# Kernel optimization log

Measured on AMD Instinct MI355X. Metric: run time of the kernel, lower is better.

## Reference

```python
import jax, jax.numpy as jnp
import numpy as np
import math

B, N, D, H = 32, 512, 512, 8
DK = D // H
MAX_DIST = 100.0
BINS = 20
BIN_SIZE = MAX_DIST / BINS


def setup_inputs() -> dict:
    key = jax.random.key(0)
    ks = jax.random.split(key, 12)
    s = 1.0 / math.sqrt(D)
    inp = {
        "x": jax.random.normal(ks[0], (B, N, D), dtype=jnp.float32),
        "distance_matrix": jax.random.uniform(ks[1], (B, N, N), dtype=jnp.float32) * MAX_DIST,
        "Wq": jax.random.uniform(ks[2], (D, D), jnp.float32, -s, s),
        "bq": jax.random.uniform(ks[3], (D,), jnp.float32, -s, s),
        "Wk": jax.random.uniform(ks[4], (D, D), jnp.float32, -s, s),
        "bk": jax.random.uniform(ks[5], (D,), jnp.float32, -s, s),
        "Wv": jax.random.uniform(ks[6], (D, D), jnp.float32, -s, s),
        "bv": jax.random.uniform(ks[7], (D,), jnp.float32, -s, s),
        "Wo": jax.random.uniform(ks[8], (D, D), jnp.float32, -s, s),
        "bo": jax.random.uniform(ks[9], (D,), jnp.float32, -s, s),
        "dist_weights": jnp.ones((BINS + 1,), dtype=jnp.float32),
    }
    return inp


def reference(x, distance_matrix, Wq, bq, Wk, bk, Wv, bv, Wo, bo, dist_weights):
    temperature = 1.0
    # Linear projections; torch nn.Linear computes x @ W.T + b
    q = (x @ Wq.T + bq).reshape(B, N, H, DK).transpose(0, 2, 1, 3)  # [B,H,N,DK]
    k = (x @ Wk.T + bk).reshape(B, N, H, DK).transpose(0, 2, 1, 3)
    v = (x @ Wv.T + bv).reshape(B, N, H, DK).transpose(0, 2, 1, 3)

    scores = jnp.einsum("bhqd,bhkd->bhqk", q, k) / math.sqrt(DK)  # [B,H,N,N]

    # Relative position bias: bin distances, look up scalar weight per pair
    binned = jnp.clip((distance_matrix / BIN_SIZE).astype(jnp.int32), 0, BINS)  # [B,N,N]
    bias = dist_weights[binned] / temperature  # [B,N,N]
    scores = scores + bias[:, None, :, :]  # broadcast over heads

    attn = jax.nn.softmax(scores, axis=-1)  # dropout is identity in eval
    out = jnp.einsum("bhqk,bhkd->bhqd", attn, v)  # [B,H,N,DK]
    out = out.transpose(0, 2, 1, 3).reshape(B, N, D)
    return out @ Wo.T + bo
```

## Files before the change

kernel.cpp:

```cpp
#include <hip/hip_runtime.h>
#include <hip/hip_fp16.h>
#include <math.h>
#include <stdint.h>

#define BB 32
#define NN 512
#define DDIM 512
#define HH 8
#define DK 64

typedef __attribute__((ext_vector_type(8))) short short8;
typedef __attribute__((ext_vector_type(4))) float floatx4;
typedef unsigned short ushort_t;
typedef unsigned int uint_t;

__device__ __forceinline__ void gl_lds16(const void* g, void* l) {
    __builtin_amdgcn_global_load_lds(
        (const __attribute__((address_space(1))) uint_t*)g,
        (__attribute__((address_space(3))) uint_t*)l,
        16, 0, 0);
}

__device__ __forceinline__ ushort_t f2bf(float f) {
    uint_t u = __builtin_bit_cast(uint_t, f);
    u += 0x7fff + ((u >> 16) & 1);
    return (ushort_t)(u >> 16);
}

__device__ __forceinline__ uint_t pkbf(float a, float b) {
    return (uint_t)f2bf(a) | ((uint_t)f2bf(b) << 16);
}

__device__ __forceinline__ float h2f(ushort_t u) {
    return __half2float(__ushort_as_half(u));
}

__global__ __launch_bounds__(256) void cvt_bf16(const float* __restrict__ s,
                                                ushort_t* __restrict__ d, int n8) {
    const int i = blockIdx.x * 256 + threadIdx.x;
    if (i >= n8) return;
    const float4 a = ((const float4*)s)[i * 2 + 0];
    const float4 b = ((const float4*)s)[i * 2 + 1];
    uint4 o;
    o.x = pkbf(a.x, a.y); o.y = pkbf(a.z, a.w);
    o.z = pkbf(b.x, b.y); o.w = pkbf(b.z, b.w);
    *(uint4*)(d + i * 8) = o;
}

__global__ __launch_bounds__(256) void cvt_w4(
    const float* __restrict__ w0, const float* __restrict__ w1,
    const float* __restrict__ w2, const float* __restrict__ w3,
    ushort_t* __restrict__ o0, ushort_t* __restrict__ o1,
    ushort_t* __restrict__ o2, ushort_t* __restrict__ o3) {
    const float* s; ushort_t* d;
    if (blockIdx.y == 0)      { s = w0; d = o0; }
    else if (blockIdx.y == 1) { s = w1; d = o1; }
    else if (blockIdx.y == 2) { s = w2; d = o2; }
    else                      { s = w3; d = o3; }
    const int i = blockIdx.x * 256 + threadIdx.x;
    const float4 a = ((const float4*)s)[i * 2 + 0];
    const float4 b = ((const float4*)s)[i * 2 + 1];
    uint4 o;
    o.x = pkbf(a.x, a.y); o.y = pkbf(a.z, a.w);
    o.z = pkbf(b.x, b.y); o.w = pkbf(b.z, b.w);
    *(uint4*)(d + i * 8) = o;
}

__global__ __launch_bounds__(256) void bias_half(const float* __restrict__ dist,
                                                 const float* __restrict__ dw,
                                                 ushort_t* __restrict__ T, int n8) {
    __shared__ float dws[21];
    if (threadIdx.x < 21) dws[threadIdx.x] = (dw[threadIdx.x] - 3.0f) * 1.44269504f;
    __syncthreads();
    const int i = blockIdx.x * 256 + threadIdx.x;
    if (i >= n8) return;
    float dv[8];
    { const float4 a = ((const float4*)dist)[i * 2 + 0];
      const float4 b = ((const float4*)dist)[i * 2 + 1];
      dv[0]=a.x; dv[1]=a.y; dv[2]=a.z; dv[3]=a.w;
      dv[4]=b.x; dv[5]=b.y; dv[6]=b.z; dv[7]=b.w; }
    ushort_t h[8];
    #pragma unroll
    for (int j = 0; j < 8; ++j) {
        int bin = (int)(dv[j] / 5.0f);
        bin = bin < 0 ? 0 : (bin > 20 ? 20 : bin);
        h[j] = __half_as_ushort(__float2half(dws[bin]));
    }
    uint4 o;
    o.x = (uint_t)h[0] | ((uint_t)h[1] << 16);
    o.y = (uint_t)h[2] | ((uint_t)h[3] << 16);
    o.z = (uint_t)h[4] | ((uint_t)h[5] << 16);
    o.w = (uint_t)h[6] | ((uint_t)h[7] << 16);
    *(uint4*)(T + i * 8) = o;
}

__global__ __launch_bounds__(256) void transp_v(const ushort_t* __restrict__ V,
                                                ushort_t* __restrict__ Vt) {
    __shared__ ushort_t T[64][72];
    const int tid = threadIdx.x;
    const int q0 = blockIdx.x * 64;
    const int bh = blockIdx.y, b = bh >> 3, h = bh & 7;
    #pragma unroll
    for (int rnd = 0; rnd < 2; ++rnd) {
        const int idx = rnd * 256 + tid;
        const int row = idx >> 3, c8 = (idx & 7) * 8;
        const uint4 v = *(const uint4*)&V[((size_t)(b * NN + q0 + row)) * DDIM + h * DK + c8];
        ushort_t* t = &T[row][c8];
        t[0] = (ushort_t)v.x; t[1] = (ushort_t)(v.x >> 16);
        t[2] = (ushort_t)v.y; t[3] = (ushort_t)(v.y >> 16);
        t[4] = (ushort_t)v.z; t[5] = (ushort_t)(v.z >> 16);
        t[6] = (ushort_t)v.w; t[7] = (ushort_t)(v.w >> 16);
    }
    __syncthreads();
    #pragma unroll
    for (int rnd = 0; rnd < 2; ++rnd) {
        const int idx = rnd * 256 + tid;
        const int d = idx >> 3, q8 = (idx & 7) * 8;
        uint4 o;
        o.x = (uint_t)T[q8 + 0][d] | ((uint_t)T[q8 + 1][d] << 16);
        o.y = (uint_t)T[q8 + 2][d] | ((uint_t)T[q8 + 3][d] << 16);
        o.z = (uint_t)T[q8 + 4][d] | ((uint_t)T[q8 + 5][d] << 16);
        o.w = (uint_t)T[q8 + 6][d] | ((uint_t)T[q8 + 7][d] << 16);
        *(uint4*)&Vt[((size_t)(bh * DK + d)) * NN + q0 + q8] = o;
    }
}

#define GEMM_CORE(Aptr, Wptr)                                                           \
    __shared__ ushort_t As[128 * 32];                                                   \
    __shared__ ushort_t Bs[128 * 32];                                                   \
    const int tid = threadIdx.x;                                                        \
    const int lane = tid & 63, wid = tid >> 6;                                          \
    const int quad = lane >> 4, l15 = lane & 15;                                        \
    const int m0 = blockIdx.x * 128, n0 = blockIdx.y * 128;                             \
    const int wy = wid >> 1, wx = wid & 1;                                              \
    floatx4 acc[4][4];                                                                  \
    _Pragma("unroll") for (int i = 0; i < 4; ++i)                                       \
        _Pragma("unroll") for (int j = 0; j < 4; ++j)                                   \
            _Pragma("unroll") for (int r = 0; r < 4; ++r) acc[i][j][r] = 0.f;           \
    for (int k0 = 0; k0 < DDIM; k0 += 32) {                                             \
        __syncthreads();                                                                \
        _Pragma("unroll") for (int j = 0; j < 4; ++j) {                                 \
            const int t = wid * 4 + j;                                                  \
            const int rowi = ((t & 7) << 4) + (lane >> 2);                              \
            const int cd = (lane & 3) ^ ((rowi >> 1) & 3);                              \
            if (t < 8)                                                                  \
                gl_lds16(Aptr + (size_t)(m0 + rowi) * DDIM + k0 + cd * 8,               \
                         (char*)As + ((t & 7) << 10));                                  \
            else                                                                        \
                gl_lds16(Wptr + (size_t)(n0 + rowi) * DDIM + k0 + cd * 8,               \
                         (char*)Bs + ((t & 7) << 10));                                  \
        }                                                                               \
        __syncthreads();                                                                \
        short8 aw[4], bt[4];                                                            \
        _Pragma("unroll") for (int fi = 0; fi < 4; ++fi) {                              \
            const int r = wy * 64 + fi * 16 + l15;                                      \
            aw[fi] = *(const short8*)((const char*)Bs + r * 64 +                        \
                                      ((quad ^ ((r >> 1) & 3)) << 4));                  \
        }                                                                               \
        _Pragma("unroll") for (int ti = 0; ti < 4; ++ti) {                              \
            const int r = wx * 64 + ti * 16 + l15;                                      \
            bt[ti] = *(const short8*)((const char*)As + r * 64 +                        \
                                      ((quad ^ ((r >> 1) & 3)) << 4));                  \
        }                                                                               \
        _Pragma("unroll") for (int fi = 0; fi < 4; ++fi)                                \
            _Pragma("unroll") for (int ti = 0; ti < 4; ++ti)                            \
                acc[fi][ti] = __builtin_amdgcn_mfma_f32_16x16x32_bf16(                  \
                    aw[fi], bt[ti], acc[fi][ti], 0, 0, 0);                              \
    }

__global__ __launch_bounds__(256) void gemm_qkv(
    const ushort_t* __restrict__ A,
    const ushort_t* __restrict__ W0, const ushort_t* __restrict__ W1,
    const ushort_t* __restrict__ W2,
    const float* __restrict__ b0, const float* __restrict__ b1,
    const float* __restrict__ b2,
    ushort_t* __restrict__ o0, ushort_t* __restrict__ o1, ushort_t* __restrict__ o2) {
    const ushort_t* W; const float* bias; ushort_t* dst;
    if (blockIdx.z == 0)      { W = W0; bias = b0; dst = o0; }
    else if (blockIdx.z == 1) { W = W1; bias = b1; dst = o1; }
    else                      { W = W2; bias = b2; dst = o2; }
    GEMM_CORE(A, W)
    #pragma unroll
    for (int fi = 0; fi < 4; ++fi) {
        const int f = n0 + wy * 64 + fi * 16 + quad * 4;
        const float4 b4 = *(const float4*)&bias[f];
        #pragma unroll
        for (int ti = 0; ti < 4; ++ti) {
            const int token = m0 + wx * 64 + ti * 16 + l15;
            uint2 v;
            v.x = pkbf(acc[fi][ti][0] + b4.x, acc[fi][ti][1] + b4.y);
            v.y = pkbf(acc[fi][ti][2] + b4.z, acc[fi][ti][3] + b4.w);
            *(uint2*)&dst[(size_t)token * DDIM + f] = v;
        }
    }
}

__global__ __launch_bounds__(256) void gemm_out(
    const ushort_t* __restrict__ A, const ushort_t* __restrict__ Wo,
    const float* __restrict__ bo, float* __restrict__ dst) {
    GEMM_CORE(A, Wo)
    #pragma unroll
    for (int fi = 0; fi < 4; ++fi) {
        const int f = n0 + wy * 64 + fi * 16 + quad * 4;
        const float4 b4 = *(const float4*)&bo[f];
        #pragma unroll
        for (int ti = 0; ti < 4; ++ti) {
            const int token = m0 + wx * 64 + ti * 16 + l15;
            float4 v;
            v.x = acc[fi][ti][0] + b4.x; v.y = acc[fi][ti][1] + b4.y;
            v.z = acc[fi][ti][2] + b4.z; v.w = acc[fi][ti][3] + b4.w;
            *(float4*)&dst[(size_t)token * DDIM + f] = v;
        }
    }
}

__global__ __launch_bounds__(256) void attn_mfma(
    const ushort_t* __restrict__ Qg, const ushort_t* __restrict__ Kg,
    const ushort_t* __restrict__ Vtg, const ushort_t* __restrict__ Tg,
    ushort_t* __restrict__ aout) {
    __shared__ ushort_t Ks[64 * 64];
    __shared__ ushort_t Vs[64 * 64];
    __shared__ ushort_t Ps[64 * 64];

    const int tid = threadIdx.x, lane = tid & 63, wid = tid >> 6;
    const int quad = lane >> 4, l15 = lane & 15;
    const int q0 = blockIdx.x * 64, h = blockIdx.y, b = blockIdx.z;
    const int qrow = q0 + wid * 16 + l15;
    const float K1 = 0.18033688f;

    const ushort_t* qp = Qg + (size_t)(b * NN + qrow) * DDIM + h * DK;
    short8 bq[2];
    #pragma unroll
    for (int ks = 0; ks < 2; ++ks)
        bq[ks] = *(const short8*)(qp + ks * 32 + quad * 8);

    const ushort_t* trow = Tg + (size_t)(b * NN + qrow) * NN;
    const int prow = wid * 16 + l15;
    const int swk = l15 & 7;

    floatx4 O[4];
    #pragma unroll
    for (int ni = 0; ni < 4; ++ni)
        #pragma unroll
        for (int r = 0; r < 4; ++r) O[ni][r] = 0.f;
    float lsum = 0.f;

    for (int kt = 0; kt < 8; ++kt) {
        const int k0 = kt * 64;
        __syncthreads();
        #pragma unroll
        for (int j = 0; j < 2; ++j) {
            const int t = wid * 2 + j;
            const int row = t * 8 + (lane >> 3);
            const int cd = (lane & 7) ^ (row & 7) ^ ((row >> 3) & 7);
            gl_lds16(Kg + (size_t)(b * NN + k0 + row) * DDIM + h * DK + cd * 8,
                     (char*)Ks + t * 1024);
            gl_lds16(Vtg + ((size_t)((b * HH + h) * DK + row)) * NN + k0 + cd * 8,
                     (char*)Vs + t * 1024);
        }
        uint2 tv[4];
        #pragma unroll
        for (int f = 0; f < 4; ++f)
            tv[f] = *(const uint2*)(trow + k0 + f * 16 + quad * 4);
        __syncthreads();

        floatx4 S[4];
        #pragma unroll
        for (int f = 0; f < 4; ++f)
            #pragma unroll
            for (int r = 0; r < 4; ++r) S[f][r] = 0.f;
        #pragma unroll
        for (int ks = 0; ks < 2; ++ks) {
            #pragma unroll
            for (int f = 0; f < 4; ++f) {
                const int r = f * 16 + l15;
                const int ch = (ks * 4 + quad) ^ (r & 7) ^ ((r >> 3) & 7);
                const short8 ak = *(const short8*)((const char*)Ks + r * 128 + (ch << 4));
                S[f] = __builtin_amdgcn_mfma_f32_16x16x32_bf16(ak, bq[ks], S[f], 0, 0, 0);
            }
        }

        #pragma unroll
        for (int f = 0; f < 4; ++f) {
            const float t0 = h2f((ushort_t)(tv[f].x));
            const float t1 = h2f((ushort_t)(tv[f].x >> 16));
            const float t2 = h2f((ushort_t)(tv[f].y));
            const float t3 = h2f((ushort_t)(tv[f].y >> 16));
            const float p0 = exp2f(S[f][0] * K1 + t0);
            const float p1 = exp2f(S[f][1] * K1 + t1);
            const float p2 = exp2f(S[f][2] * K1 + t2);
            const float p3 = exp2f(S[f][3] * K1 + t3);
            lsum += (p0 + p1) + (p2 + p3);
            uint2 pw;
            pw.x = pkbf(p0, p1);
            pw.y = pkbf(p2, p3);
            *(uint2*)((char*)Ps + prow * 128 + (((f * 4 + quad) ^ (swk << 1)) << 3)) = pw;
        }

        #pragma unroll
        for (int ks = 0; ks < 2; ++ks) {
            const int chp = ((ks * 4 + quad) ^ swk) << 4;
            const short8 bp = *(const short8*)((const char*)Ps + prow * 128 + chp);
            #pragma unroll
            for (int ni = 0; ni < 4; ++ni) {
                const int rv = ni * 16 + l15;
                const int chv = (ks * 4 + quad) ^ (rv & 7) ^ ((rv >> 3) & 7);
                const short8 av = *(const short8*)((const char*)Vs + rv * 128 + (chv << 4));
                O[ni] = __builtin_amdgcn_mfma_f32_16x16x32_bf16(av, bp, O[ni], 0, 0, 0);
            }
        }
    }

    lsum += __shfl_xor(lsum, 16);
    lsum += __shfl_xor(lsum, 32);
    const float inv = 1.0f / lsum;
    #pragma unroll
    for (int ni = 0; ni < 4; ++ni) {
        uint2 ov;
        ov.x = pkbf(O[ni][0] * inv, O[ni][1] * inv);
        ov.y = pkbf(O[ni][2] * inv, O[ni][3] * inv);
        *(uint2*)&aout[(size_t)(b * NN + qrow) * DDIM + h * DK + ni * 16 + quad * 4] = ov;
    }
}

extern "C" void kernel_launch(void* const* d_in, const int* in_sizes, int n_in,
                              void* d_out, int out_size, void* d_ws, size_t ws_size,
                              hipStream_t stream) {
    const float* x    = (const float*)d_in[0];
    const float* dist = (const float*)d_in[1];
    const float* Wq   = (const float*)d_in[2];
    const float* bq   = (const float*)d_in[3];
    const float* Wk   = (const float*)d_in[4];
    const float* bk   = (const float*)d_in[5];
    const float* Wv   = (const float*)d_in[6];
    const float* bv   = (const float*)d_in[7];
    const float* Wo   = (const float*)d_in[8];
    const float* bo   = (const float*)d_in[9];
    const float* dw   = (const float*)d_in[10];
    float* out = (float*)d_out;

    const size_t NELT = (size_t)BB * NN * DDIM;
    ushort_t* xb  = (ushort_t*)d_ws;
    ushort_t* wqb = xb + NELT;
    ushort_t* wkb = wqb + DDIM * DDIM;
    ushort_t* wvb = wkb + DDIM * DDIM;
    ushort_t* wob = wvb + DDIM * DDIM;
    ushort_t* qb  = wob + DDIM * DDIM;
    ushort_t* kb  = qb + NELT;
    ushort_t* vb  = kb + NELT;
    ushort_t* vt  = vb + NELT;
    ushort_t* Tm  = vt + NELT;
    ushort_t* ab  = xb;

    cvt_bf16<<<4096, 256, 0, stream>>>(x, xb, (int)(NELT / 8));
    cvt_w4<<<dim3(128, 4), 256, 0, stream>>>(Wq, Wk, Wv, Wo, wqb, wkb, wvb, wob);
    bias_half<<<4096, 256, 0, stream>>>(dist, dw, Tm, (int)(NELT / 8));

    gemm_qkv<<<dim3(128, 4, 3), 256, 0, stream>>>(xb, wqb, wkb, wvb, bq, bk, bv,
                                                  qb, kb, vb);
    transp_v<<<dim3(8, 256), 256, 0, stream>>>(vb, vt);
    attn_mfma<<<dim3(8, 8, 32), 256, 0, stream>>>(qb, kb, vt, Tm, ab);
    gemm_out<<<dim3(128, 4), 256, 0, stream>>>(ab, wob, bo, out);
}
```

Before: 250.0 us.

## Fuse attention per batch-head with full K/V resident in LDS and fp16 PV

Rewrites attention so each block handles one (batch, head) with 512 threads, loading all K and transposed V into shared memory once, then each wave processes 64 queries without per-tile barriers. V projection output and softmax probabilities switch to fp16 so the PV product uses f16 MFMA. This removes redundant K/V reloads and synchronisation across query tiles, at the cost of large LDS use (one block per CU), high register pressure, and an unoverlapped upfront load.

Measured after the change: 245.8 us. No clear change (-1.7%).

```diff
diff --git a/kernel.cpp b/kernel.cpp
--- a/kernel.cpp
+++ b/kernel.cpp
@@ -10,6 +10,8 @@
 #define DK 64
 
 typedef __attribute__((ext_vector_type(8))) short short8;
+typedef __attribute__((ext_vector_type(8))) _Float16 half8;
+typedef __attribute__((ext_vector_type(2))) _Float16 half2v;
 typedef __attribute__((ext_vector_type(4))) float floatx4;
 typedef unsigned short ushort_t;
 typedef unsigned int uint_t;
@@ -29,6 +31,10 @@
 
 __device__ __forceinline__ uint_t pkbf(float a, float b) {
     return (uint_t)f2bf(a) | ((uint_t)f2bf(b) << 16);
+}
+
+__device__ __forceinline__ uint_t pkh(float a, float b) {
+    return __builtin_bit_cast(uint_t, __builtin_amdgcn_cvt_pkrtz(a, b));
 }
 
 __device__ __forceinline__ float h2f(ushort_t u) {
@@ -179,6 +185,7 @@
     if (blockIdx.z == 0)      { W = W0; bias = b0; dst = o0; }
     else if (blockIdx.z == 1) { W = W1; bias = b1; dst = o1; }
     else                      { W = W2; bias = b2; dst = o2; }
+    const bool as_f16 = (blockIdx.z == 2);
     GEMM_CORE(A, W)
     #pragma unroll
     for (int fi = 0; fi < 4; ++fi) {
@@ -187,9 +194,11 @@
         #pragma unroll
         for (int ti = 0; ti < 4; ++ti) {
             const int token = m0 + wx * 64 + ti * 16 + l15;
+            const float v0 = acc[fi][ti][0] + b4.x, v1 = acc[fi][ti][1] + b4.y;
+            const float v2 = acc[fi][ti][2] + b4.z, v3 = acc[fi][ti][3] + b4.w;
             uint2 v;
-            v.x = pkbf(acc[fi][ti][0] + b4.x, acc[fi][ti][1] + b4.y);
-            v.y = pkbf(acc[fi][ti][2] + b4.z, acc[fi][ti][3] + b4.w);
+            if (as_f16) { v.x = pkh(v0, v1);  v.y = pkh(v2, v3); }
+            else        { v.x = pkbf(v0, v1); v.y = pkbf(v2, v3); }
             *(uint2*)&dst[(size_t)token * DDIM + f] = v;
         }
     }
@@ -214,112 +223,152 @@
     }
 }
 
-__global__ __launch_bounds__(256) void attn_mfma(
+__global__ __launch_bounds__(512, 2) void attn_fused(
     const ushort_t* __restrict__ Qg, const ushort_t* __restrict__ Kg,
     const ushort_t* __restrict__ Vtg, const ushort_t* __restrict__ Tg,
     ushort_t* __restrict__ aout) {
-    __shared__ ushort_t Ks[64 * 64];
-    __shared__ ushort_t Vs[64 * 64];
-    __shared__ ushort_t Ps[64 * 64];
+    __shared__ ushort_t Ks[512 * 64];
+    __shared__ ushort_t Vs[64 * 512];
+    __shared__ ushort_t Ps[8 * 1024];
 
     const int tid = threadIdx.x, lane = tid & 63, wid = tid >> 6;
     const int quad = lane >> 4, l15 = lane & 15;
-    const int q0 = blockIdx.x * 64, h = blockIdx.y, b = blockIdx.z;
-    const int qrow = q0 + wid * 16 + l15;
+    const int h = blockIdx.x, b = blockIdx.y;
     const float K1 = 0.18033688f;
 
-    const ushort_t* qp = Qg + (size_t)(b * NN + qrow) * DDIM + h * DK;
-    short8 bq[2];
-    #pragma unroll
-    for (int ks = 0; ks < 2; ++ks)
-        bq[ks] = *(const short8*)(qp + ks * 32 + quad * 8);
-
-    const ushort_t* trow = Tg + (size_t)(b * NN + qrow) * NN;
-    const int prow = wid * 16 + l15;
+    #pragma unroll
+    for (int j = 0; j < 8; ++j) {
+        const int t = wid * 8 + j;
+        {
+            const int row = t * 8 + (lane >> 3);
+            const int key = (row & 7) ^ ((row >> 3) & 7);
+            const int g = (lane & 7) ^ key;
+            gl_lds16(Kg + (size_t)(b * NN + row) * DDIM + h * DK + g * 8,
+                     (char*)Ks + t * 1024);
+        }
+        {
+            const int key = (t & 7) ^ ((t >> 3) & 7);
+            const int g = lane ^ key;
+            gl_lds16(Vtg + (size_t)((b * HH + h) * DK + t) * NN + g * 8,
+                     (char*)Vs + t * 1024);
+        }
+    }
+
+    short8 bq[4][2];
+    #pragma unroll
+    for (int qs = 0; qs < 4; ++qs) {
+        const ushort_t* qp =
+            Qg + (size_t)(b * NN + wid * 64 + qs * 16 + l15) * DDIM + h * DK;
+        bq[qs][0] = *(const short8*)(qp + quad * 8);
+        bq[qs][1] = *(const short8*)(qp + 32 + quad * 8);
+    }
+
+    float lsum[4] = {0.f, 0.f, 0.f, 0.f};
+    floatx4 O[4][4];
+    #pragma unroll
+    for (int qs = 0; qs < 4; ++qs)
+        #pragma unroll
+        for (int ni = 0; ni < 4; ++ni)
+            #pragma unroll
+            for (int r = 0; r < 4; ++r) O[qs][ni][r] = 0.f;
+
+    char* const pbase = (char*)Ps + wid * 2048;
     const int swk = l15 & 7;
 
-    floatx4 O[4];
-    #pragma unroll
-    for (int ni = 0; ni < 4; ++ni)
-        #pragma unroll
-        for (int r = 0; r < 4; ++r) O[ni][r] = 0.f;
-    float lsum = 0.f;
+    __syncthreads();
 
     for (int kt = 0; kt < 8; ++kt) {
-        const int k0 = kt * 64;
-        __syncthreads();
-        #pragma unroll
-        for (int j = 0; j < 2; ++j) {
-            const int t = wid * 2 + j;
-            const int row = t * 8 + (lane >> 3);
-            const int cd = (lane & 7) ^ (row & 7) ^ ((row >> 3) & 7);
-            gl_lds16(Kg + (size_t)(b * NN + k0 + row) * DDIM + h * DK + cd * 8,
-                     (char*)Ks + t * 1024);
-            gl_lds16(Vtg + ((size_t)((b * HH + h) * DK + row)) * NN + k0 + cd * 8,
-                     (char*)Vs + t * 1024);
-        }
-        uint2 tv[4];
-        #pragma unroll
-        for (int f = 0; f < 4; ++f)
-            tv[f] = *(const uint2*)(trow + k0 + f * 16 + quad * 4);
-        __syncthreads();
-
-        floatx4 S[4];
-        #pragma unroll
-        for (int f = 0; f < 4; ++f)
-            #pragma unroll
-            for (int r = 0; r < 4; ++r) S[f][r] = 0.f;
-        #pragma unroll
-        for (int ks = 0; ks < 2; ++ks) {
+        uint2 tv[4][4];
+        #pragma unroll
+        for (int qs = 0; qs < 4; ++qs) {
+            const ushort_t* tp =
+                Tg + (size_t)(b * NN + wid * 64 + qs * 16 + l15) * NN + kt * 64;
+            #pragma unroll
+            for (int f = 0; f < 4; ++f)
+                tv[qs][f] = *(const uint2*)(tp + f * 16 + quad * 4);
+        }
+        short8 kf[2][4];
+        #pragma unroll
+        for (int ks = 0; ks < 2; ++ks)
             #pragma unroll
             for (int f = 0; f < 4; ++f) {
-                const int r = f * 16 + l15;
-                const int ch = (ks * 4 + quad) ^ (r & 7) ^ ((r >> 3) & 7);
-                const short8 ak = *(const short8*)((const char*)Ks + r * 128 + (ch << 4));
-                S[f] = __builtin_amdgcn_mfma_f32_16x16x32_bf16(ak, bq[ks], S[f], 0, 0, 0);
+                const int row = kt * 64 + f * 16 + l15;
+                const int key = (row & 7) ^ ((row >> 3) & 7);
+                kf[ks][f] = *(const short8*)((const char*)Ks + row * 128 +
+                                             (((ks * 4 + quad) ^ key) << 4));
             }
-        }
-
-        #pragma unroll
-        for (int f = 0; f < 4; ++f) {
-            const float t0 = h2f((ushort_t)(tv[f].x));
-            const float t1 = h2f((ushort_t)(tv[f].x >> 16));
-            const float t2 = h2f((ushort_t)(tv[f].y));
-            const float t3 = h2f((ushort_t)(tv[f].y >> 16));
-            const float p0 = exp2f(S[f][0] * K1 + t0);
-            const float p1 = exp2f(S[f][1] * K1 + t1);
-            const float p2 = exp2f(S[f][2] * K1 + t2);
-            const float p3 = exp2f(S[f][3] * K1 + t3);
-            lsum += (p0 + p1) + (p2 + p3);
-            uint2 pw;
-            pw.x = pkbf(p0, p1);
-            pw.y = pkbf(p2, p3);
-            *(uint2*)((char*)Ps + prow * 128 + (((f * 4 + quad) ^ (swk << 1)) << 3)) = pw;
-        }
-
-        #pragma unroll
-        for (int ks = 0; ks < 2; ++ks) {
-            const int chp = ((ks * 4 + quad) ^ swk) << 4;
-            const short8 bp = *(const short8*)((const char*)Ps + prow * 128 + chp);
+        half8 vf[2][4];
+        #pragma unroll
+        for (int ks = 0; ks < 2; ++ks)
             #pragma unroll
             for (int ni = 0; ni < 4; ++ni) {
-                const int rv = ni * 16 + l15;
-                const int chv = (ks * 4 + quad) ^ (rv & 7) ^ ((rv >> 3) & 7);
-                const short8 av = *(const short8*)((const char*)Vs + rv * 128 + (chv << 4));
-                O[ni] = __builtin_amdgcn_mfma_f32_16x16x32_bf16(av, bp, O[ni], 0, 0, 0);
+                const int d = ni * 16 + l15;
+                const int key = (d & 7) ^ ((d >> 3) & 7);
+                const int c = (kt * 8 + ks * 4 + quad) ^ key;
+                vf[ks][ni] = *(const half8*)((const char*)Vs + d * 1024 + (c << 4));
             }
-        }
-    }
-
-    lsum += __shfl_xor(lsum, 16);
-    lsum += __shfl_xor(lsum, 32);
-    const float inv = 1.0f / lsum;
-    #pragma unroll
-    for (int ni = 0; ni < 4; ++ni) {
-        uint2 ov;
-        ov.x = pkbf(O[ni][0] * inv, O[ni][1] * inv);
-        ov.y = pkbf(O[ni][2] * inv, O[ni][3] * inv);
-        *(uint2*)&aout[(size_t)(b * NN + qrow) * DDIM + h * DK + ni * 16 + quad * 4] = ov;
+
+        #pragma unroll
+        for (int qs = 0; qs < 4; ++qs) {
+            floatx4 S[4];
+            #pragma unroll
+            for (int f = 0; f < 4; ++f)
+                #pragma unroll
+                for (int r = 0; r < 4; ++r) S[f][r] = 0.f;
+            #pragma unroll
+            for (int ks = 0; ks < 2; ++ks)
+                #pragma unroll
+                for (int f = 0; f < 4; ++f)
+                    S[f] = __builtin_amdgcn_mfma_f32_16x16x32_bf16(
+                        kf[ks][f], bq[qs][ks], S[f], 0, 0, 0);
+
+            float ls = 0.f;
+            #pragma unroll
+            for (int f = 0; f < 4; ++f) {
+                const float t0 = h2f((ushort_t)(tv[qs][f].x));
+                const float t1 = h2f((ushort_t)(tv[qs][f].x >> 16));
+                const float t2 = h2f((ushort_t)(tv[qs][f].y));
+                const float t3 = h2f((ushort_t)(tv[qs][f].y >> 16));
+                const float p0 = exp2f(S[f][0] * K1 + t0);
+                const float p1 = exp2f(S[f][1] * K1 + t1);
+                const float p2 = exp2f(S[f][2] * K1 + t2);
+                const float p3 = exp2f(S[f][3] * K1 + t3);
+                ls += (p0 + p1) + (p2 + p3);
+                uint2 pw;
+                pw.x = pkh(p0, p1);
+                pw.y = pkh(p2, p3);
+                *(uint2*)(pbase + l15 * 128 +
+                          (((f * 4 + quad) ^ (swk << 1)) << 3)) = pw;
+            }
+            lsum[qs] += ls;
+
+            #pragma unroll
+            for (int ks = 0; ks < 2; ++ks) {
+                const half8 bp = *(const half8*)(pbase + l15 * 128 +
+                                                 (((ks * 4 + quad) ^ swk) << 4));
+                #pragma unroll
+                for (int ni = 0; ni < 4; ++ni)
+                    O[qs][ni] = __builtin_amdgcn_mfma_f32_16x16x32_f16(
+                        vf[ks][ni], bp, O[qs][ni], 0, 0, 0);
+            }
+        }
+    }
+
+    #pragma unroll
+    for (int qs = 0; qs < 4; ++qs) {
+        float l = lsum[qs];
+        l += __shfl_xor(l, 16);
+        l += __shfl_xor(l, 32);
+        const float inv = 1.0f / l;
+        const size_t orow =
+            (size_t)(b * NN + wid * 64 + qs * 16 + l15) * DDIM + h * DK;
+        #pragma unroll
+        for (int ni = 0; ni < 4; ++ni) {
+            uint2 ov;
+            ov.x = pkbf(O[qs][ni][0] * inv, O[qs][ni][1] * inv);
+            ov.y = pkbf(O[qs][ni][2] * inv, O[qs][ni][3] * inv);
+            *(uint2*)&aout[orow + ni * 16 + quad * 4] = ov;
+        }
     }
 }
 
@@ -359,6 +408,6 @@
     gemm_qkv<<<dim3(128, 4, 3), 256, 0, stream>>>(xb, wqb, wkb, wvb, bq, bk, bv,
                                                   qb, kb, vb);
     transp_v<<<dim3(8, 256), 256, 0, stream>>>(vb, vt);
-    attn_mfma<<<dim3(8, 8, 32), 256, 0, stream>>>(qb, kb, vt, Tm, ab);
+    attn_fused<<<dim3(HH, BB), 512, 0, stream>>>(qb, kb, vt, Tm, ab);
     gemm_out<<<dim3(128, 4), 256, 0, stream>>>(ab, wob, bo, out);
 }
```
